# Performance work log

Hardware: AMD Instinct MI355X
Metric: run time of the kernel (lower is better)

Reference implementation:

```python
import jax, jax.numpy as jnp
import numpy as np

B, S, D, F, E, K = 2, 1024, 2048, 1024, 8, 2


def setup_inputs() -> dict:
    key = jax.random.key(0)
    ks = jax.random.split(key, 5)
    scale_x = 0.02
    return {
        "x": jax.random.normal(ks[0], (B, S, D), dtype=jnp.float32),
        "w_router": jax.random.normal(ks[1], (E, D), dtype=jnp.float32) * scale_x,
        "w_gate": jax.random.normal(ks[2], (E, F, D), dtype=jnp.float32) * scale_x,
        "w_up": jax.random.normal(ks[3], (E, F, D), dtype=jnp.float32) * scale_x,
        "w_down": jax.random.normal(ks[4], (E, D, F), dtype=jnp.float32) * scale_x,
        "top_k": K,
    }


def reference(x, w_router, w_gate, w_up, w_down, top_k):
    # Router: logits [B,S,E] -> top-k indices + softmax over top-k logits (fp32)
    logits = jnp.einsum("bsd,ed->bse", x, w_router)
    top_logits, top_idx = jax.lax.top_k(logits, top_k)          # [B,S,K]
    gates = jax.nn.softmax(top_logits.astype(jnp.float32), axis=-1)
    # SwitchGLU: per-expert gated MLP. Compute all experts densely, then gather
    # the selected expert output per token (reference-faithful math).
    h = jax.nn.silu(jnp.einsum("bsd,efd->besf", x, w_gate)) * jnp.einsum(
        "bsd,efd->besf", x, w_up
    )                                                            # [B,E,S,F]
    out_all = jnp.einsum("besf,edf->bsed", h, w_down)            # [B,S,E,D]
    y = jnp.take_along_axis(out_all, top_idx[..., None], axis=2)  # [B,S,K,D]
    return (y * gates[..., None].astype(y.dtype)).sum(axis=-2)   # [B,S,D]
```

## Files before the change

kernel.cpp:

```cpp
#include <hip/hip_runtime.h>
#include <hip/hip_bf16.h>

#define T_TOK 2048
#define DIM   2048
#define FFN   1024
#define NE    8

typedef __attribute__((ext_vector_type(8))) short bf16x8;
typedef __attribute__((ext_vector_type(4))) float f32x4;

__device__ __forceinline__ unsigned short f2bf(float f) {
  __hip_bfloat16 h = __float2bfloat16(f);
  return __builtin_bit_cast(unsigned short, h);
}

__device__ __forceinline__ void gload_lds16(const unsigned short* g, unsigned short* l) {
  __builtin_amdgcn_global_load_lds(
      (const __attribute__((address_space(1))) void*)g,
      (__attribute__((address_space(3))) void*)l, 16, 0, 0);
}

__global__ void cvt_f32_to_bf16(const float* __restrict__ in,
                                unsigned short* __restrict__ out, int n4) {
  int i = blockIdx.x * blockDim.x + threadIdx.x;
  int stride = gridDim.x * blockDim.x;
  for (; i < n4; i += stride) {
    float4 v = reinterpret_cast<const float4*>(in)[i];
    ushort4 o;
    o.x = f2bf(v.x); o.y = f2bf(v.y); o.z = f2bf(v.z); o.w = f2bf(v.w);
    reinterpret_cast<ushort4*>(out)[i] = o;
  }
}

__global__ __launch_bounds__(256) void router_topk(
    const float* __restrict__ x, const float* __restrict__ wr,
    int* __restrict__ top_i, float* __restrict__ top_g) {
  int t = blockIdx.x * 4 + (threadIdx.x >> 6);
  int lane = threadIdx.x & 63;
  const float4* xr = reinterpret_cast<const float4*>(x) + (size_t)t * (DIM / 4);
  const float4* wrv = reinterpret_cast<const float4*>(wr);
  float acc[NE];
#pragma unroll
  for (int e = 0; e < NE; ++e) acc[e] = 0.f;
#pragma unroll
  for (int it = 0; it < DIM / 4 / 64; ++it) {
    int d4 = it * 64 + lane;
    float4 xv = xr[d4];
#pragma unroll
    for (int e = 0; e < NE; ++e) {
      float4 wv = wrv[e * (DIM / 4) + d4];
      acc[e] += xv.x * wv.x + xv.y * wv.y + xv.z * wv.z + xv.w * wv.w;
    }
  }
#pragma unroll
  for (int off = 32; off > 0; off >>= 1) {
#pragma unroll
    for (int e = 0; e < NE; ++e) acc[e] += __shfl_xor(acc[e], off, 64);
  }
  if (lane == 0) {
    int i0 = 0; float m0 = acc[0];
#pragma unroll
    for (int e = 1; e < NE; ++e) if (acc[e] > m0) { m0 = acc[e]; i0 = e; }
    int i1 = -1; float m1 = -3.4e38f;
#pragma unroll
    for (int e = 0; e < NE; ++e) if (e != i0 && acc[e] > m1) { m1 = acc[e]; i1 = e; }
    float tv = expf(m1 - m0);
    float den = 1.f + tv;
    top_i[t * 2 + 0] = i0; top_i[t * 2 + 1] = i1;
    top_g[t * 2 + 0] = 1.f / den; top_g[t * 2 + 1] = tv / den;
  }
}

__global__ void count_offsets(const int* __restrict__ top_i,
                              int* __restrict__ offs, int* __restrict__ cursor) {
  __shared__ int cnt[NE];
  if (threadIdx.x < NE) cnt[threadIdx.x] = 0;
  __syncthreads();
  for (int i = threadIdx.x; i < T_TOK * 2; i += blockDim.x) atomicAdd(&cnt[top_i[i]], 1);
  __syncthreads();
  if (threadIdx.x == 0) {
    int s = 0;
    for (int e = 0; e < NE; ++e) { offs[e] = s; cursor[e] = s; s += cnt[e]; }
    offs[NE] = s;
  }
}

__global__ void scatter_tokens(const int* __restrict__ top_i, const float* __restrict__ top_g,
                               int* __restrict__ cursor, int* __restrict__ tok_list,
                               float* __restrict__ gate_lst, int* __restrict__ slot_lst) {
  int t = blockIdx.x * blockDim.x + threadIdx.x;
  if (t >= T_TOK) return;
#pragma unroll
  for (int s = 0; s < 2; ++s) {
    int e = top_i[t * 2 + s];
    int p = atomicAdd(&cursor[e], 1);
    tok_list[p] = t;
    gate_lst[p] = top_g[t * 2 + s];
    slot_lst[p] = s;
  }
}

__global__ __launch_bounds__(256, 2) void gateup_gemm(
    const unsigned short* __restrict__ xb, const unsigned short* __restrict__ wgb,
    const unsigned short* __restrict__ wub, const int* __restrict__ tok_list,
    const int* __restrict__ offs, unsigned short* __restrict__ hbuf) {
  const int e = blockIdx.z;
  const int row0 = offs[e];
  const int n_e = offs[e + 1] - row0;
  const int mt = blockIdx.y;
  if (mt * 128 >= n_e) return;
  const int nt = blockIdx.x;

  __shared__ unsigned short As[128 * 32];
  __shared__ unsigned short Bg[128 * 32];
  __shared__ unsigned short Bu[128 * 32];

  const int tid = threadIdx.x;
  const int wid = tid >> 6;
  const int lane = tid & 63;

  const int sr0 = wid * 32 + (lane >> 2);
  const int sr1 = sr0 + 16;
  const int sc = (lane & 3) * 8;

  int ar0 = mt * 128 + sr0; if (ar0 >= n_e) ar0 = n_e - 1;
  int ar1 = mt * 128 + sr1; if (ar1 >= n_e) ar1 = n_e - 1;
  const unsigned short* ga0 = xb + (size_t)tok_list[row0 + ar0] * DIM + sc;
  const unsigned short* ga1 = xb + (size_t)tok_list[row0 + ar1] * DIM + sc;

  const size_t wbase = (size_t)e * FFN * DIM + (size_t)(nt * 128) * DIM;
  const unsigned short* gg0 = wgb + wbase + (size_t)sr0 * DIM + sc;
  const unsigned short* gg1 = wgb + wbase + (size_t)sr1 * DIM + sc;
  const unsigned short* gu0 = wub + wbase + (size_t)sr0 * DIM + sc;
  const unsigned short* gu1 = wub + wbase + (size_t)sr1 * DIM + sc;

  unsigned short* lA0 = &As[(wid * 32) * 32];
  unsigned short* lA1 = &As[(wid * 32 + 16) * 32];
  unsigned short* lG0 = &Bg[(wid * 32) * 32];
  unsigned short* lG1 = &Bg[(wid * 32 + 16) * 32];
  unsigned short* lU0 = &Bu[(wid * 32) * 32];
  unsigned short* lU1 = &Bu[(wid * 32 + 16) * 32];

  f32x4 accg[4][4];
  f32x4 accu[4][4];
#pragma unroll
  for (int i = 0; i < 4; ++i)
#pragma unroll
    for (int j = 0; j < 4; ++j) {
      accg[i][j] = (f32x4){0.f, 0.f, 0.f, 0.f};
      accu[i][j] = (f32x4){0.f, 0.f, 0.f, 0.f};
    }

  const int wrow = (wid >> 1) * 64;
  const int wcol = (wid & 1) * 64;
  const int frow = lane & 15;
  const int fk = (lane >> 4) * 8;

  for (int k0 = 0; k0 < DIM; k0 += 32) {
    gload_lds16(ga0 + k0, lA0);
    gload_lds16(ga1 + k0, lA1);
    gload_lds16(gg0 + k0, lG0);
    gload_lds16(gg1 + k0, lG1);
    gload_lds16(gu0 + k0, lU0);
    gload_lds16(gu1 + k0, lU1);
    __syncthreads();
    bf16x8 af[4], bg[4], bu[4];
#pragma unroll
    for (int i = 0; i < 4; ++i)
      af[i] = *reinterpret_cast<const bf16x8*>(&As[(wrow + i * 16 + frow) * 32 + fk]);
#pragma unroll
    for (int j = 0; j < 4; ++j) {
      bg[j] = *reinterpret_cast<const bf16x8*>(&Bg[(wcol + j * 16 + frow) * 32 + fk]);
      bu[j] = *reinterpret_cast<const bf16x8*>(&Bu[(wcol + j * 16 + frow) * 32 + fk]);
    }
#pragma unroll
    for (int i = 0; i < 4; ++i)
#pragma unroll
      for (int j = 0; j < 4; ++j) {
        accg[i][j] = __builtin_amdgcn_mfma_f32_16x16x32_bf16(af[i], bg[j], accg[i][j], 0, 0, 0);
        accu[i][j] = __builtin_amdgcn_mfma_f32_16x16x32_bf16(af[i], bu[j], accu[i][j], 0, 0, 0);
      }
    __syncthreads();
  }

#pragma unroll
  for (int i = 0; i < 4; ++i) {
#pragma unroll
    for (int jj = 0; jj < 4; ++jj) {
      int r = mt * 128 + wrow + i * 16 + (lane >> 4) * 4 + jj;
      if (r < n_e) {
#pragma unroll
        for (int j = 0; j < 4; ++j) {
          float g = accg[i][j][jj];
          float u = accu[i][j][jj];
          float h = (g / (1.f + __expf(-g))) * u;
          int f = nt * 128 + wcol + j * 16 + (lane & 15);
          hbuf[(size_t)(row0 + r) * FFN + f] = f2bf(h);
        }
      }
    }
  }
}

__global__ __launch_bounds__(256, 2) void down_gemm(
    const unsigned short* __restrict__ hbuf, const unsigned short* __restrict__ wdb,
    const int* __restrict__ tok_list, const float* __restrict__ gate_lst,
    const int* __restrict__ slot_lst, const int* __restrict__ offs,
    float* __restrict__ yslots) {
  const int e = blockIdx.z;
  const int row0 = offs[e];
  const int n_e = offs[e + 1] - row0;
  const int mt = blockIdx.y;
  if (mt * 128 >= n_e) return;
  const int nt = blockIdx.x;

  __shared__ unsigned short As[128 * 32];
  __shared__ unsigned short Bs[128 * 32];

  const int tid = threadIdx.x;
  const int wid = tid >> 6;
  const int lane = tid & 63;

  const int sr0 = wid * 32 + (lane >> 2);
  const int sr1 = sr0 + 16;
  const int sc = (lane & 3) * 8;

  int ar0 = mt * 128 + sr0; if (ar0 >= n_e) ar0 = n_e - 1;
  int ar1 = mt * 128 + sr1; if (ar1 >= n_e) ar1 = n_e - 1;
  const unsigned short* ga0 = hbuf + (size_t)(row0 + ar0) * FFN + sc;
  const unsigned short* ga1 = hbuf + (size_t)(row0 + ar1) * FFN + sc;

  const unsigned short* gb0 = wdb + ((size_t)e * DIM + nt * 128 + sr0) * FFN + sc;
  const unsigned short* gb1 = wdb + ((size_t)e * DIM + nt * 128 + sr1) * FFN + sc;

  unsigned short* lA0 = &As[(wid * 32) * 32];
  unsigned short* lA1 = &As[(wid * 32 + 16) * 32];
  unsigned short* lB0 = &Bs[(wid * 32) * 32];
  unsigned short* lB1 = &Bs[(wid * 32 + 16) * 32];

  f32x4 acc[4][4];
#pragma unroll
  for (int i = 0; i < 4; ++i)
#pragma unroll
    for (int j = 0; j < 4; ++j) acc[i][j] = (f32x4){0.f, 0.f, 0.f, 0.f};

  const int wrow = (wid >> 1) * 64;
  const int wcol = (wid & 1) * 64;
  const int frow = lane & 15;
  const int fk = (lane >> 4) * 8;

  for (int k0 = 0; k0 < FFN; k0 += 32) {
    gload_lds16(ga0 + k0, lA0);
    gload_lds16(ga1 + k0, lA1);
    gload_lds16(gb0 + k0, lB0);
    gload_lds16(gb1 + k0, lB1);
    __syncthreads();
    bf16x8 af[4], bf[4];
#pragma unroll
    for (int i = 0; i < 4; ++i)
      af[i] = *reinterpret_cast<const bf16x8*>(&As[(wrow + i * 16 + frow) * 32 + fk]);
#pragma unroll
    for (int j = 0; j < 4; ++j)
      bf[j] = *reinterpret_cast<const bf16x8*>(&Bs[(wcol + j * 16 + frow) * 32 + fk]);
#pragma unroll
    for (int i = 0; i < 4; ++i)
#pragma unroll
      for (int j = 0; j < 4; ++j)
        acc[i][j] = __builtin_amdgcn_mfma_f32_16x16x32_bf16(af[i], bf[j], acc[i][j], 0, 0, 0);
    __syncthreads();
  }

#pragma unroll
  for (int i = 0; i < 4; ++i) {
#pragma unroll
    for (int jj = 0; jj < 4; ++jj) {
      int r = mt * 128 + wrow + i * 16 + (lane >> 4) * 4 + jj;
      if (r < n_e) {
        int tk = tok_list[row0 + r];
        float gt = gate_lst[row0 + r];
        int sl = slot_lst[row0 + r];
        float* yrow = yslots + ((size_t)sl * T_TOK + tk) * DIM;
#pragma unroll
        for (int j = 0; j < 4; ++j) {
          int d = nt * 128 + wcol + j * 16 + (lane & 15);
          yrow[d] = gt * acc[i][j][jj];
        }
      }
    }
  }
}

__global__ void combine(const float* __restrict__ y, float* __restrict__ out) {
  int i = blockIdx.x * blockDim.x + threadIdx.x;
  int stride = gridDim.x * blockDim.x;
  const float4* y0 = reinterpret_cast<const float4*>(y);
  const float4* y1 = reinterpret_cast<const float4*>(y + (size_t)T_TOK * DIM);
  float4* o = reinterpret_cast<float4*>(out);
  for (; i < T_TOK * DIM / 4; i += stride) {
    float4 a = y0[i], b = y1[i];
    float4 r;
    r.x = a.x + b.x; r.y = a.y + b.y; r.z = a.z + b.z; r.w = a.w + b.w;
    o[i] = r;
  }
}

extern "C" void kernel_launch(void* const* d_in, const int* in_sizes, int n_in,
                              void* d_out, int out_size, void* d_ws, size_t ws_size,
                              hipStream_t stream) {
  const float* x = (const float*)d_in[0];
  const float* wr = (const float*)d_in[1];
  const float* wg = (const float*)d_in[2];
  const float* wu = (const float*)d_in[3];
  const float* wd = (const float*)d_in[4];
  float* out = (float*)d_out;

  char* ws = (char*)d_ws;
  size_t off = 0;
  auto alloc = [&](size_t bytes) {
    char* p = ws + off;
    off += (bytes + 255) & ~(size_t)255;
    return p;
  };
  unsigned short* xb   = (unsigned short*)alloc((size_t)T_TOK * DIM * 2);
  unsigned short* wgb  = (unsigned short*)alloc((size_t)NE * FFN * DIM * 2);
  unsigned short* wub  = (unsigned short*)alloc((size_t)NE * FFN * DIM * 2);
  unsigned short* wdb  = (unsigned short*)alloc((size_t)NE * DIM * FFN * 2);
  unsigned short* hbuf = (unsigned short*)alloc((size_t)T_TOK * 2 * FFN * 2);
  float* yslots        = (float*)alloc((size_t)2 * T_TOK * DIM * 4);
  int* top_i     = (int*)alloc(T_TOK * 2 * 4);
  float* top_g   = (float*)alloc(T_TOK * 2 * 4);
  int* tok_list  = (int*)alloc(T_TOK * 2 * 4);
  float* gate_lst = (float*)alloc(T_TOK * 2 * 4);
  int* slot_lst  = (int*)alloc(T_TOK * 2 * 4);
  int* offs      = (int*)alloc(64);
  int* cursor    = (int*)alloc(64);
  if (off > ws_size) return;

  cvt_f32_to_bf16<<<2048, 256, 0, stream>>>(x, xb, T_TOK * DIM / 4);
  cvt_f32_to_bf16<<<4096, 256, 0, stream>>>(wg, wgb, NE * FFN * DIM / 4);
  cvt_f32_to_bf16<<<4096, 256, 0, stream>>>(wu, wub, NE * FFN * DIM / 4);
  cvt_f32_to_bf16<<<4096, 256, 0, stream>>>(wd, wdb, NE * DIM * FFN / 4);
  router_topk<<<T_TOK / 4, 256, 0, stream>>>(x, wr, top_i, top_g);
  count_offsets<<<1, 256, 0, stream>>>(top_i, offs, cursor);
  scatter_tokens<<<(T_TOK + 255) / 256, 256, 0, stream>>>(top_i, top_g, cursor, tok_list,
                                                          gate_lst, slot_lst);
  gateup_gemm<<<dim3(FFN / 128, T_TOK / 128, NE), 256, 0, stream>>>(xb, wgb, wub, tok_list,
                                                                    offs, hbuf);
  down_gemm<<<dim3(DIM / 128, T_TOK / 128, NE), 256, 0, stream>>>(hbuf, wdb, tok_list, gate_lst,
                                                                  slot_lst, offs, yslots);
  combine<<<2048, 256, 0, stream>>>(yslots, out);
}
```

Before: 226.8 us.

## Shrink MoE GEMM M-tile to 64, widen K-step to 64 with XOR-swizzled LDS

Both expert GEMMs now use 64-row token tiles instead of 128, doubling the M-grid, so experts with few tokens waste less padded work and more blocks are available. The K step per LDS stage grows from 32 to 64, halving the number of barrier pairs, and the LDS layout uses an XOR swizzle on 16-byte chunks to avoid bank conflicts on fragment reads. down_gemm also asks for 4 blocks per CU. The cost is less B-tile reuse per block, so weight traffic per token rises, plus more LDS per block.

Measured after the change: 207.5 us. 8.5% less time.

```diff
diff --git a/kernel.cpp b/kernel.cpp
--- a/kernel.cpp
+++ b/kernel.cpp
@@ -108,93 +108,101 @@
   const int row0 = offs[e];
   const int n_e = offs[e + 1] - row0;
   const int mt = blockIdx.y;
-  if (mt * 128 >= n_e) return;
+  if (mt * 64 >= n_e) return;
   const int nt = blockIdx.x;
 
-  __shared__ unsigned short As[128 * 32];
-  __shared__ unsigned short Bg[128 * 32];
-  __shared__ unsigned short Bu[128 * 32];
+  __shared__ unsigned short As[64 * 64];
+  __shared__ unsigned short Bg[128 * 64];
+  __shared__ unsigned short Bu[128 * 64];
 
   const int tid = threadIdx.x;
   const int wid = tid >> 6;
   const int lane = tid & 63;
 
-  const int sr0 = wid * 32 + (lane >> 2);
-  const int sr1 = sr0 + 16;
-  const int sc = (lane & 3) * 8;
-
-  int ar0 = mt * 128 + sr0; if (ar0 >= n_e) ar0 = n_e - 1;
-  int ar1 = mt * 128 + sr1; if (ar1 >= n_e) ar1 = n_e - 1;
-  const unsigned short* ga0 = xb + (size_t)tok_list[row0 + ar0] * DIM + sc;
-  const unsigned short* ga1 = xb + (size_t)tok_list[row0 + ar1] * DIM + sc;
-
+  const int gchunk = (((lane & 7) ^ ((lane >> 3) & 7)) << 3);
+
+  const unsigned short* gA[2];
+  unsigned short* lA[2];
+#pragma unroll
+  for (int p = 0; p < 2; ++p) {
+    int rt = wid * 16 + p * 8 + (lane >> 3);
+    int ar = mt * 64 + rt; if (ar >= n_e) ar = n_e - 1;
+    gA[p] = xb + (size_t)tok_list[row0 + ar] * DIM + gchunk;
+    lA[p] = &As[(wid * 16 + p * 8) * 64];
+  }
   const size_t wbase = (size_t)e * FFN * DIM + (size_t)(nt * 128) * DIM;
-  const unsigned short* gg0 = wgb + wbase + (size_t)sr0 * DIM + sc;
-  const unsigned short* gg1 = wgb + wbase + (size_t)sr1 * DIM + sc;
-  const unsigned short* gu0 = wub + wbase + (size_t)sr0 * DIM + sc;
-  const unsigned short* gu1 = wub + wbase + (size_t)sr1 * DIM + sc;
-
-  unsigned short* lA0 = &As[(wid * 32) * 32];
-  unsigned short* lA1 = &As[(wid * 32 + 16) * 32];
-  unsigned short* lG0 = &Bg[(wid * 32) * 32];
-  unsigned short* lG1 = &Bg[(wid * 32 + 16) * 32];
-  unsigned short* lU0 = &Bu[(wid * 32) * 32];
-  unsigned short* lU1 = &Bu[(wid * 32 + 16) * 32];
-
-  f32x4 accg[4][4];
-  f32x4 accu[4][4];
-#pragma unroll
-  for (int i = 0; i < 4; ++i)
+  const unsigned short* gG[4];
+  const unsigned short* gU[4];
+  unsigned short* lG[4];
+  unsigned short* lU[4];
+#pragma unroll
+  for (int p = 0; p < 4; ++p) {
+    int rt = wid * 32 + p * 8 + (lane >> 3);
+    gG[p] = wgb + wbase + (size_t)rt * DIM + gchunk;
+    gU[p] = wub + wbase + (size_t)rt * DIM + gchunk;
+    lG[p] = &Bg[(wid * 32 + p * 8) * 64];
+    lU[p] = &Bu[(wid * 32 + p * 8) * 64];
+  }
+
+  f32x4 accg[2][4];
+  f32x4 accu[2][4];
+#pragma unroll
+  for (int i = 0; i < 2; ++i)
 #pragma unroll
     for (int j = 0; j < 4; ++j) {
       accg[i][j] = (f32x4){0.f, 0.f, 0.f, 0.f};
       accu[i][j] = (f32x4){0.f, 0.f, 0.f, 0.f};
     }
 
-  const int wrow = (wid >> 1) * 64;
-  const int wcol = (wid & 1) * 64;
+  const int warow = (wid >> 1) * 32;
+  const int wacol = (wid & 1) * 64;
   const int frow = lane & 15;
-  const int fk = (lane >> 4) * 8;
-
-  for (int k0 = 0; k0 < DIM; k0 += 32) {
-    gload_lds16(ga0 + k0, lA0);
-    gload_lds16(ga1 + k0, lA1);
-    gload_lds16(gg0 + k0, lG0);
-    gload_lds16(gg1 + k0, lG1);
-    gload_lds16(gu0 + k0, lU0);
-    gload_lds16(gu1 + k0, lU1);
+  const int eo0 = ((((0 << 2) + (lane >> 4)) ^ (lane & 7)) << 3);
+  const int eo1 = ((((1 << 2) + (lane >> 4)) ^ (lane & 7)) << 3);
+
+  for (int k0 = 0; k0 < DIM; k0 += 64) {
+#pragma unroll
+    for (int p = 0; p < 2; ++p) gload_lds16(gA[p] + k0, lA[p]);
+#pragma unroll
+    for (int p = 0; p < 4; ++p) gload_lds16(gG[p] + k0, lG[p]);
+#pragma unroll
+    for (int p = 0; p < 4; ++p) gload_lds16(gU[p] + k0, lU[p]);
     __syncthreads();
-    bf16x8 af[4], bg[4], bu[4];
-#pragma unroll
-    for (int i = 0; i < 4; ++i)
-      af[i] = *reinterpret_cast<const bf16x8*>(&As[(wrow + i * 16 + frow) * 32 + fk]);
-#pragma unroll
-    for (int j = 0; j < 4; ++j) {
-      bg[j] = *reinterpret_cast<const bf16x8*>(&Bg[(wcol + j * 16 + frow) * 32 + fk]);
-      bu[j] = *reinterpret_cast<const bf16x8*>(&Bu[(wcol + j * 16 + frow) * 32 + fk]);
-    }
-#pragma unroll
-    for (int i = 0; i < 4; ++i)
+#pragma unroll
+    for (int kk = 0; kk < 2; ++kk) {
+      const int eo = kk ? eo1 : eo0;
+      bf16x8 af[2], bg[4], bu[4];
+#pragma unroll
+      for (int i = 0; i < 2; ++i)
+        af[i] = *reinterpret_cast<const bf16x8*>(&As[(warow + i * 16 + frow) * 64 + eo]);
 #pragma unroll
       for (int j = 0; j < 4; ++j) {
-        accg[i][j] = __builtin_amdgcn_mfma_f32_16x16x32_bf16(af[i], bg[j], accg[i][j], 0, 0, 0);
-        accu[i][j] = __builtin_amdgcn_mfma_f32_16x16x32_bf16(af[i], bu[j], accu[i][j], 0, 0, 0);
+        bg[j] = *reinterpret_cast<const bf16x8*>(&Bg[(wacol + j * 16 + frow) * 64 + eo]);
+        bu[j] = *reinterpret_cast<const bf16x8*>(&Bu[(wacol + j * 16 + frow) * 64 + eo]);
       }
+#pragma unroll
+      for (int i = 0; i < 2; ++i)
+#pragma unroll
+        for (int j = 0; j < 4; ++j) {
+          accg[i][j] = __builtin_amdgcn_mfma_f32_16x16x32_bf16(af[i], bg[j], accg[i][j], 0, 0, 0);
+          accu[i][j] = __builtin_amdgcn_mfma_f32_16x16x32_bf16(af[i], bu[j], accu[i][j], 0, 0, 0);
+        }
+    }
     __syncthreads();
   }
 
 #pragma unroll
-  for (int i = 0; i < 4; ++i) {
+  for (int i = 0; i < 2; ++i) {
 #pragma unroll
     for (int jj = 0; jj < 4; ++jj) {
-      int r = mt * 128 + wrow + i * 16 + (lane >> 4) * 4 + jj;
+      int r = mt * 64 + warow + i * 16 + (lane >> 4) * 4 + jj;
       if (r < n_e) {
 #pragma unroll
         for (int j = 0; j < 4; ++j) {
           float g = accg[i][j][jj];
           float u = accu[i][j][jj];
           float h = (g / (1.f + __expf(-g))) * u;
-          int f = nt * 128 + wcol + j * 16 + (lane & 15);
+          int f = nt * 128 + wacol + j * 16 + (lane & 15);
           hbuf[(size_t)(row0 + r) * FFN + f] = f2bf(h);
         }
       }
@@ -202,7 +210,7 @@
   }
 }
 
-__global__ __launch_bounds__(256, 2) void down_gemm(
+__global__ __launch_bounds__(256, 4) void down_gemm(
     const unsigned short* __restrict__ hbuf, const unsigned short* __restrict__ wdb,
     const int* __restrict__ tok_list, const float* __restrict__ gate_lst,
     const int* __restrict__ slot_lst, const int* __restrict__ offs,
@@ -211,70 +219,78 @@
   const int row0 = offs[e];
   const int n_e = offs[e + 1] - row0;
   const int mt = blockIdx.y;
-  if (mt * 128 >= n_e) return;
+  if (mt * 64 >= n_e) return;
   const int nt = blockIdx.x;
 
-  __shared__ unsigned short As[128 * 32];
-  __shared__ unsigned short Bs[128 * 32];
+  __shared__ unsigned short As[64 * 64];
+  __shared__ unsigned short Bs[128 * 64];
 
   const int tid = threadIdx.x;
   const int wid = tid >> 6;
   const int lane = tid & 63;
 
-  const int sr0 = wid * 32 + (lane >> 2);
-  const int sr1 = sr0 + 16;
-  const int sc = (lane & 3) * 8;
-
-  int ar0 = mt * 128 + sr0; if (ar0 >= n_e) ar0 = n_e - 1;
-  int ar1 = mt * 128 + sr1; if (ar1 >= n_e) ar1 = n_e - 1;
-  const unsigned short* ga0 = hbuf + (size_t)(row0 + ar0) * FFN + sc;
-  const unsigned short* ga1 = hbuf + (size_t)(row0 + ar1) * FFN + sc;
-
-  const unsigned short* gb0 = wdb + ((size_t)e * DIM + nt * 128 + sr0) * FFN + sc;
-  const unsigned short* gb1 = wdb + ((size_t)e * DIM + nt * 128 + sr1) * FFN + sc;
-
-  unsigned short* lA0 = &As[(wid * 32) * 32];
-  unsigned short* lA1 = &As[(wid * 32 + 16) * 32];
-  unsigned short* lB0 = &Bs[(wid * 32) * 32];
-  unsigned short* lB1 = &Bs[(wid * 32 + 16) * 32];
-
-  f32x4 acc[4][4];
-#pragma unroll
-  for (int i = 0; i < 4; ++i)
+  const int gchunk = (((lane & 7) ^ ((lane >> 3) & 7)) << 3);
+
+  const unsigned short* gA[2];
+  unsigned short* lA[2];
+#pragma unroll
+  for (int p = 0; p < 2; ++p) {
+    int rt = wid * 16 + p * 8 + (lane >> 3);
+    int ar = mt * 64 + rt; if (ar >= n_e) ar = n_e - 1;
+    gA[p] = hbuf + (size_t)(row0 + ar) * FFN + gchunk;
+    lA[p] = &As[(wid * 16 + p * 8) * 64];
+  }
+  const unsigned short* gB[4];
+  unsigned short* lB[4];
+#pragma unroll
+  for (int p = 0; p < 4; ++p) {
+    int rt = wid * 32 + p * 8 + (lane >> 3);
+    gB[p] = wdb + ((size_t)e * DIM + nt * 128 + rt) * FFN + gchunk;
+    lB[p] = &Bs[(wid * 32 + p * 8) * 64];
+  }
+
+  f32x4 acc[2][4];
+#pragma unroll
+  for (int i = 0; i < 2; ++i)
 #pragma unroll
     for (int j = 0; j < 4; ++j) acc[i][j] = (f32x4){0.f, 0.f, 0.f, 0.f};
 
-  const int wrow = (wid >> 1) * 64;
-  const int wcol = (wid & 1) * 64;
+  const int warow = (wid >> 1) * 32;
+  const int wacol = (wid & 1) * 64;
   const int frow = lane & 15;
-  const int fk = (lane >> 4) * 8;
-
-  for (int k0 = 0; k0 < FFN; k0 += 32) {
-    gload_lds16(ga0 + k0, lA0);
-    gload_lds16(ga1 + k0, lA1);
-    gload_lds16(gb0 + k0, lB0);
-    gload_lds16(gb1 + k0, lB1);
+  const int eo0 = ((((0 << 2) + (lane >> 4)) ^ (lane & 7)) << 3);
+  const int eo1 = ((((1 << 2) + (lane >> 4)) ^ (lane & 7)) << 3);
+
+  for (int k0 = 0; k0 < FFN; k0 += 64) {
+#pragma unroll
+    for (int p = 0; p < 2; ++p) gload_lds16(gA[p] + k0, lA[p]);
+#pragma unroll
+    for (int p = 0; p < 4; ++p) gload_lds16(gB[p] + k0, lB[p]);
     __syncthreads();
-    bf16x8 af[4], bf[4];
-#pragma unroll
-    for (int i = 0; i < 4; ++i)
-      af[i] = *reinterpret_cast<const bf16x8*>(&As[(wrow + i * 16 + frow) * 32 + fk]);
-#pragma unroll
-    for (int j = 0; j < 4; ++j)
-      bf[j] = *reinterpret_cast<const bf16x8*>(&Bs[(wcol + j * 16 + frow) * 32 + fk]);
-#pragma unroll
-    for (int i = 0; i < 4; ++i)
+#pragma unroll
+    for (int kk = 0; kk < 2; ++kk) {
+      const int eo = kk ? eo1 : eo0;
+      bf16x8 af[2], bf[4];
+#pragma unroll
+      for (int i = 0; i < 2; ++i)
+        af[i] = *reinterpret_cast<const bf16x8*>(&As[(warow + i * 16 + frow) * 64 + eo]);
 #pragma unroll
       for (int j = 0; j < 4; ++j)
-        acc[i][j] = __builtin_amdgcn_mfma_f32_16x16x32_bf16(af[i], bf[j], acc[i][j], 0, 0, 0);
+        bf[j] = *reinterpret_cast<const bf16x8*>(&Bs[(wacol + j * 16 + frow) * 64 + eo]);
+#pragma unroll
+      for (int i = 0; i < 2; ++i)
+#pragma unroll
+        for (int j = 0; j < 4; ++j)
+          acc[i][j] = __builtin_amdgcn_mfma_f32_16x16x32_bf16(af[i], bf[j], acc[i][j], 0, 0, 0);
+    }
     __syncthreads();
   }
 
 #pragma unroll
-  for (int i = 0; i < 4; ++i) {
+  for (int i = 0; i < 2; ++i) {
 #pragma unroll
     for (int jj = 0; jj < 4; ++jj) {
-      int r = mt * 128 + wrow + i * 16 + (lane >> 4) * 4 + jj;
+      int r = mt * 64 + warow + i * 16 + (lane >> 4) * 4 + jj;
       if (r < n_e) {
         int tk = tok_list[row0 + r];
         float gt = gate_lst[row0 + r];
@@ -282,7 +298,7 @@
         float* yrow = yslots + ((size_t)sl * T_TOK + tk) * DIM;
 #pragma unroll
         for (int j = 0; j < 4; ++j) {
-          int d = nt * 128 + wcol + j * 16 + (lane & 15);
+          int d = nt * 128 + wacol + j * 16 + (lane & 15);
           yrow[d] = gt * acc[i][j][jj];
         }
       }
@@ -344,9 +360,8 @@
   count_offsets<<<1, 256, 0, stream>>>(top_i, offs, cursor);
   scatter_tokens<<<(T_TOK + 255) / 256, 256, 0, stream>>>(top_i, top_g, cursor, tok_list,
                                                           gate_lst, slot_lst);
-  gateup_gemm<<<dim3(FFN / 128, T_TOK / 128, NE), 256, 0, stream>>>(xb, wgb, wub, tok_list,
-                                                                    offs, hbuf);
-  down_gemm<<<dim3(DIM / 128, T_TOK / 128, NE), 256, 0, stream>>>(hbuf, wdb, tok_list, gate_lst,
-                                                                  slot_lst, offs, yslots);
+  gateup_gemm<<<dim3(FFN / 128, 32, NE), 256, 0, stream>>>(xb, wgb, wub, tok_list, offs, hbuf);
+  down_gemm<<<dim3(DIM / 128, 32, NE), 256, 0, stream>>>(hbuf, wdb, tok_list, gate_lst,
+                                                         slot_lst, offs, yslots);
   combine<<<2048, 256, 0, stream>>>(yslots, out);
 }
```
